# Kernel tuning notes

Measured on AMD Instinct MI355X. Metric: run time of the kernel, lower is better.

The kernel has to match this reference:

```python
import jax, jax.numpy as jnp
import numpy as np

HIDDEN = 1024
NUM_EXPERTS = 16
TOP_K = 6
EPS = 1e-10


def setup_inputs() -> dict:
    key = jax.random.key(0)
    k1, k2, k3, k4 = jax.random.split(key, 4)
    tokens = jax.random.normal(k1, (4, 2048, HIDDEN), dtype=jnp.float32)
    # torch.nn.Linear(hidden_size, num_experts): weight [E, H], bias [E]
    bound = 1.0 / np.sqrt(HIDDEN)
    router_w = jax.random.uniform(k2, (NUM_EXPERTS, HIDDEN), jnp.float32, -bound, bound)
    router_b = jax.random.uniform(k3, (NUM_EXPERTS,), jnp.float32, -bound, bound)
    # expert_weights = randn(E, H, H) / sqrt(H)
    expert_w = jax.random.normal(k4, (NUM_EXPERTS, HIDDEN, HIDDEN), dtype=jnp.float32) / np.sqrt(HIDDEN)
    return {"tokens": tokens, "router_w": router_w, "router_b": router_b, "expert_w": expert_w}


def reference(tokens, router_w, router_b, expert_w):
    B, S, H = tokens.shape
    E = expert_w.shape[0]
    T = B * S

    # Router: softmax -> top-k -> renormalize top-k probs
    logits = jnp.einsum("bsh,eh->bse", tokens, router_w) + router_b  # [B,S,E]
    probs = jax.nn.softmax(logits, axis=-1)
    top_p, top_i = jax.lax.top_k(probs, TOP_K)                        # [B,S,K]
    top_p = top_p / (jnp.sum(top_p, axis=-1, keepdims=True) + EPS)

    x = tokens.reshape(T, H)
    flat_i = top_i.reshape(T, TOP_K)
    flat_p = top_p.reshape(T, TOP_K)

    # Dense gate matrix [T, E]: scatter of normalized top-k weights.
    # Equivalent to the expand/sort/pad + weighted scatter-add restore.
    gate = jnp.zeros((T, E), dtype=flat_p.dtype)
    gate = gate.at[jnp.arange(T)[:, None], flat_i].add(flat_p)
    acc = jnp.maximum(jnp.sum(gate, axis=-1), EPS)  # weight accumulator (clamp min=1e-10)

    # Grouped GEMM equivalent: per-expert matmul weighted by gate, accumulated.
    out = jnp.zeros_like(x)
    for e in range(E):  # fixed, small structural loop over experts
        out = out + (x @ expert_w[e]) * gate[:, e:e + 1]
    out = (out / acc[:, None]).reshape(B, S, H)

    # 'dummy' gradient-connection term from restore_output_with_triton_and_gradients
    out = out + EPS * jnp.sum(top_p, axis=-1, keepdims=True)
    return out
```

## Files before the change

kernel.cpp:

```cpp
#include <hip/hip_runtime.h>
#include <cstdint>
#include <cstddef>

#define NE 16
#define TOPK 6
#define HID 1024
#define NTOK 8192
#define EPSF 1e-10f
#define CAP_ROWS 51200
#define MAXB256 208
#define NT 16
#define ROUTER_BLKS 2048

typedef short bf16x8 __attribute__((ext_vector_type(8)));
typedef float f32x4 __attribute__((ext_vector_type(4)));

__device__ __forceinline__ unsigned int f2bf_rne(float f) {
  union { float f; unsigned int u; } v;
  v.f = f;
  return (v.u + 0x7FFFu + ((v.u >> 16) & 1u)) >> 16;
}

__device__ __forceinline__ float bfbits2f(unsigned int hi16) {
  union { unsigned int u; float f; } v;
  v.u = hi16 << 16;
  return v.f;
}

__device__ __forceinline__ void load_lds16(const void* g, void* l) {
  __builtin_amdgcn_global_load_lds(
      (const __attribute__((address_space(1))) void*)g,
      (__attribute__((address_space(3))) void*)l, 16, 0, 0);
}

__global__ __launch_bounds__(256) void fused_pre_kernel(
    const float* __restrict__ tokens, const float* __restrict__ rw,
    const float* __restrict__ rb, unsigned short* __restrict__ Xb,
    unsigned int* __restrict__ topk, float* __restrict__ g6,
    float* __restrict__ epst, const float* __restrict__ ew,
    unsigned short* __restrict__ wt) {
  __shared__ float tile[64][65];
  const int tid = threadIdx.x;
  const unsigned bx = blockIdx.x;

  if (bx >= ROUTER_BLKS) {
    const int q = bx - ROUTER_BLKS;
    const int e2 = q >> 8;
    const int ntile = ((q >> 4) & 15) * 64;
    const int ktile = (q & 15) * 64;
    const int tr = tid >> 6;
    const int tc = tid & 63;
    const float* wp = ew + (size_t)e2 * HID * HID;
#pragma unroll
    for (int r = 0; r < 64; r += 4)
      tile[r + tr][tc] = wp[(size_t)(ktile + r + tr) * HID + ntile + tc];
    __syncthreads();
    unsigned short* wo = wt + (size_t)e2 * HID * HID;
    const int aa = tid & 31;
    const int rg = tid >> 5;
#pragma unroll
    for (int c2 = 0; c2 < 64; c2 += 8) {
      const int n = c2 + rg;
      const unsigned lo = f2bf_rne(tile[2 * aa][n]);
      const unsigned hi = f2bf_rne(tile[2 * aa + 1][n]);
      *(unsigned int*)(wo + (size_t)(ntile + n) * HID + ktile + 2 * aa) =
          lo | (hi << 16);
    }
    return;
  }

  const int wv = tid >> 6;
  const int lane = tid & 63;
  const int token = (int)bx * 4 + wv;

  const float4* xp4 = (const float4*)(tokens + (size_t)token * HID);
  float4 x4[4];
#pragma unroll
  for (int j = 0; j < 4; ++j) x4[j] = xp4[lane + 64 * j];

  unsigned short* xbrow = Xb + (size_t)token * HID;
#pragma unroll
  for (int j = 0; j < 4; ++j) {
    const unsigned lo = f2bf_rne(x4[j].x) | (f2bf_rne(x4[j].y) << 16);
    const unsigned hi = f2bf_rne(x4[j].z) | (f2bf_rne(x4[j].w) << 16);
    *(uint2*)(xbrow + 4 * (lane + 64 * j)) = (uint2){lo, hi};
  }

  float lg[NE];
#pragma unroll
  for (int e = 0; e < NE; ++e) {
    const float4* wp4 = (const float4*)(rw + e * HID);
    float p = 0.f;
#pragma unroll
    for (int j = 0; j < 4; ++j) {
      const float4 w = wp4[lane + 64 * j];
      p += x4[j].x * w.x + x4[j].y * w.y + x4[j].z * w.z + x4[j].w * w.w;
    }
    lg[e] = p;
  }
#pragma unroll
  for (int m = 1; m < 64; m <<= 1) {
#pragma unroll
    for (int e = 0; e < NE; ++e) lg[e] += __shfl_xor(lg[e], m);
  }
  float mx = -1e30f;
#pragma unroll
  for (int e = 0; e < NE; ++e) {
    lg[e] += rb[e];
    mx = fmaxf(mx, lg[e]);
  }
  float q[NE];
  float s_all = 0.f;
#pragma unroll
  for (int e = 0; e < NE; ++e) {
    q[e] = expf(lg[e] - mx);
    s_all += q[e];
  }
  unsigned sel = 0, pack = 0;
  float s_top = 0.f;
  float gq[TOPK];
#pragma unroll
  for (int k = 0; k < TOPK; ++k) {
    float best = -1.f;
    int bi = 0;
#pragma unroll
    for (int e = 0; e < NE; ++e) {
      bool taken = (sel >> e) & 1u;
      if (!taken && q[e] > best) { best = q[e]; bi = e; }
    }
    sel |= 1u << bi;
    gq[k] = best;
    s_top += best;
    pack |= ((unsigned)bi) << (4 * k);
  }
  if (lane < TOPK)
    g6[(size_t)token * TOPK + lane] = gq[lane] / s_top;
  if (lane == 32) {
    topk[token] = pack;
    float s = s_top / s_all;
    epst[token] = EPSF * (s / (s + EPSF));
  }
}

__global__ __launch_bounds__(1024) void sortassign_kernel(
    const unsigned int* __restrict__ topk, const float* __restrict__ g6,
    unsigned int* __restrict__ tokmap, float* __restrict__ gpos,
    unsigned int* __restrict__ inv, unsigned int* __restrict__ table,
    unsigned int* __restrict__ total) {
  __shared__ unsigned int sred[NE][65];
  __shared__ unsigned int s_seg[NE];
  __shared__ unsigned int hist[NE];
  __shared__ unsigned int s_sc[1024];
  const int e = blockIdx.x;
  const int tid = threadIdx.x;

  {
    const unsigned hx = tid & 15u;
    const int hc = tid >> 4;
    const unsigned int* tp = topk + hc * 128;
    unsigned hcnt = 0;
    for (int i = 0; i < 128; ++i) {
      const unsigned p = tp[i];
#pragma unroll
      for (int k = 0; k < TOPK; ++k) hcnt += (((p >> (4 * k)) & 15u) == hx);
    }
    sred[hx][hc] = hcnt;
  }
  __syncthreads();
  if (tid < NE) {
    unsigned s = 0;
    for (int j = 0; j < 64; ++j) s += sred[tid][j];
    hist[tid] = s;
  }
  __syncthreads();
  if (tid == 0) {
    unsigned off = 0;
    for (int i = 0; i < NE; ++i) {
      s_seg[i] = off;
      off += ((hist[i] + 127) >> 7) << 7;
    }
  }
  __syncthreads();
  if (e == 0 && tid == 0) {
    unsigned b = 0;
    for (int i = 0; i < NE; ++i) {
      const unsigned nb = (hist[i] + 127) >> 7;
      const unsigned seg = s_seg[i];
      unsigned m = 0;
      for (; m + 2 <= nb; m += 2)
        table[b++] = ((unsigned)i << 24) | (seg + m * 128);
      if (m < nb)
        table[b++] = ((unsigned)i << 24) | (1u << 23) | (seg + m * 128);
    }
    *total = b;
  }

  const int tbase = tid * (NTOK / 1024);
  unsigned c = 0;
  for (int i = 0; i < NTOK / 1024; ++i) {
    const unsigned p = topk[tbase + i];
#pragma unroll
    for (int k = 0; k < TOPK; ++k) c += (((p >> (4 * k)) & 15u) == (unsigned)e);
  }
  s_sc[tid] = c;
  __syncthreads();
  for (int off = 1; off < 1024; off <<= 1) {
    unsigned v = (tid >= off) ? s_sc[tid - off] : 0u;
    __syncthreads();
    s_sc[tid] += v;
    __syncthreads();
  }
  const unsigned seg0 = s_seg[e];
  unsigned pos = seg0 + s_sc[tid] - c;
  for (int i = 0; i < NTOK / 1024; ++i) {
    const int t = tbase + i;
    const unsigned p = topk[t];
#pragma unroll
    for (int k = 0; k < TOPK; ++k) {
      if (((p >> (4 * k)) & 15u) == (unsigned)e) {
        tokmap[pos] = (unsigned)t;
        gpos[pos] = g6[(size_t)t * TOPK + k];
        inv[(size_t)t * TOPK + k] = pos;
        ++pos;
      }
    }
  }
  const unsigned cnt_e = s_sc[1023];
  const unsigned segend = seg0 + (((cnt_e + 127) >> 7) << 7);
  for (unsigned p2 = seg0 + cnt_e + tid; p2 < segend; p2 += 1024) {
    tokmap[p2] = 0u;
    gpos[p2] = 0.f;
  }
}

__global__ __launch_bounds__(512, 2) void moe_ggemm_kernel(
    const unsigned short* __restrict__ Xb, const unsigned short* __restrict__ Wt,
    const unsigned int* __restrict__ table, const unsigned int* __restrict__ total,
    const unsigned int* __restrict__ tokmap, const float* __restrict__ gpos,
    unsigned short* __restrict__ Y) {
  __shared__ unsigned short As[2][256][64];
  __shared__ unsigned short Bs[2][256][64];
  __shared__ unsigned int Ts[256];
  __shared__ float Gs[256];

  const unsigned tot = *total;
  const unsigned bx = blockIdx.x;
  const unsigned wg = (bx & 7u) * (MAXB256 * 4u / 8u) + (bx >> 3);
  const unsigned slot = wg >> 2;
  if (slot >= tot) return;
  const int n0 = (int)(wg & 3u) * 256;
  const unsigned ent = table[slot];
  const int e = (int)(ent >> 24);
  const int half = (int)((ent >> 23) & 1u);
  const int row0 = (int)(ent & 0x7FFFFFu);

  const int tid = threadIdx.x;
  const int wv = tid >> 6;
  const int lane = tid & 63;
  const int lm = lane & 15;
  const int quad = lane >> 4;
  const int wvm = wv >> 2;
  const int woff_m = wvm * 128;
  const int woff_n = (wv & 3) * 64;

  if (tid < 256) {
    const int rc = (half && tid >= 128) ? 127 : tid;
    Ts[tid] = tokmap[row0 + rc];
    Gs[tid] = (half && tid >= 128) ? 0.f : gpos[row0 + rc];
  }
  __syncthreads();

  const int srow = tid >> 3;
  const int scol = ((tid & 7) ^ (srow & 7)) << 4;
  const char* pA[4];
  const char* pB[4];
#pragma unroll
  for (int i = 0; i < 4; ++i) {
    pA[i] = (const char*)Xb + (size_t)Ts[i * 64 + srow] * (HID * 2) + scol;
    pB[i] = (const char*)Wt + (size_t)e * (HID * HID * 2) +
            (size_t)(n0 + i * 64 + srow) * (HID * 2) + scol;
  }
  char* const Ab = (char*)&As[0][0][0];
  char* const Bb = (char*)&Bs[0][0][0];
  const int sdst = wv * 8 * 128;

  load_lds16(pA[0], Ab + 0 * 8192 + sdst);
  load_lds16(pA[2], Ab + 2 * 8192 + sdst);
  load_lds16(pB[0], Bb + 0 * 8192 + sdst);
  load_lds16(pB[1], Bb + 1 * 8192 + sdst);
  load_lds16(pB[2], Bb + 2 * 8192 + sdst);
  load_lds16(pB[3], Bb + 3 * 8192 + sdst);
  load_lds16(pA[1], Ab + 1 * 8192 + sdst);
  load_lds16(pA[3], Ab + 3 * 8192 + sdst);

  f32x4 acc[8][4];
#pragma unroll
  for (int f = 0; f < 8; ++f)
#pragma unroll
    for (int g = 0; g < 4; ++g) acc[f][g] = (f32x4){0.f, 0.f, 0.f, 0.f};

  const int rsw = (lm & 7) << 4;
  const int roff0 = (quad * 16) ^ rsw;
  const int roff1 = (64 + quad * 16) ^ rsw;

  asm volatile("s_waitcnt vmcnt(2)" ::: "memory");
  __builtin_amdgcn_s_barrier();

  for (int kt = 0; kt < NT; ++kt) {
    const int c = kt & 1;
    const int koff = (kt < NT - 1 ? kt + 1 : kt) * 128;
    const char* ab = Ab + c * 32768;
    const char* bb = Bb + c * 32768;
    char* const ast = Ab + (c ^ 1) * 32768;
    char* const bst = Bb + (c ^ 1) * 32768;

    bf16x8 a[4][2], b[4][2];

#pragma unroll
    for (int f = 0; f < 4; ++f) {
      const char* rp = ab + (woff_m + 16 * f + lm) * 128;
      a[f][0] = *(const bf16x8*)(rp + roff0);
      a[f][1] = *(const bf16x8*)(rp + roff1);
    }
#pragma unroll
    for (int g = 0; g < 2; ++g) {
      const char* rp = bb + (woff_n + 16 * g + lm) * 128;
      b[g][0] = *(const bf16x8*)(rp + roff0);
      b[g][1] = *(const bf16x8*)(rp + roff1);
    }
    load_lds16(pA[0] + koff, ast + 0 * 8192 + sdst);
    load_lds16(pA[2] + koff, ast + 2 * 8192 + sdst);
    __builtin_amdgcn_s_barrier();
    asm volatile("s_waitcnt lgkmcnt(0)" ::: "memory");
    __builtin_amdgcn_s_setprio(1);
#pragma unroll
    for (int f = 0; f < 4; ++f)
#pragma unroll
      for (int g = 0; g < 2; ++g) {
        acc[f][g] = __builtin_amdgcn_mfma_f32_16x16x32_bf16(a[f][0], b[g][0], acc[f][g], 0, 0, 0);
        acc[f][g] = __builtin_amdgcn_mfma_f32_16x16x32_bf16(a[f][1], b[g][1], acc[f][g], 0, 0, 0);
      }
    __builtin_amdgcn_s_setprio(0);
    __builtin_amdgcn_s_barrier();

#pragma unroll
    for (int g = 2; g < 4; ++g) {
      const char* rp = bb + (woff_n + 16 * g + lm) * 128;
      b[g][0] = *(const bf16x8*)(rp + roff0);
      b[g][1] = *(const bf16x8*)(rp + roff1);
    }
    load_lds16(pB[0] + koff, bst + 0 * 8192 + sdst);
    load_lds16(pB[1] + koff, bst + 1 * 8192 + sdst);
    __builtin_amdgcn_s_barrier();
    asm volatile("s_waitcnt lgkmcnt(0)" ::: "memory");
    __builtin_amdgcn_s_setprio(1);
#pragma unroll
    for (int f = 0; f < 4; ++f)
#pragma unroll
      for (int g = 2; g < 4; ++g) {
        acc[f][g] = __builtin_amdgcn_mfma_f32_16x16x32_bf16(a[f][0], b[g][0], acc[f][g], 0, 0, 0);
        acc[f][g] = __builtin_amdgcn_mfma_f32_16x16x32_bf16(a[f][1], b[g][1], acc[f][g], 0, 0, 0);
      }
    __builtin_amdgcn_s_setprio(0);
    asm volatile("s_waitcnt vmcnt(4)" ::: "memory");
    __builtin_amdgcn_s_barrier();

#pragma unroll
    for (int f = 0; f < 4; ++f) {
      const char* rp = ab + (woff_m + 16 * (f + 4) + lm) * 128;
      a[f][0] = *(const bf16x8*)(rp + roff0);
      a[f][1] = *(const bf16x8*)(rp + roff1);
    }
    load_lds16(pB[2] + koff, bst + 2 * 8192 + sdst);
    load_lds16(pB[3] + koff, bst + 3 * 8192 + sdst);
    __builtin_amdgcn_s_barrier();
    asm volatile("s_waitcnt lgkmcnt(0)" ::: "memory");
    __builtin_amdgcn_s_setprio(1);
#pragma unroll
    for (int f = 0; f < 4; ++f)
#pragma unroll
      for (int g = 2; g < 4; ++g) {
        acc[f + 4][g] = __builtin_amdgcn_mfma_f32_16x16x32_bf16(a[f][0], b[g][0], acc[f + 4][g], 0, 0, 0);
        acc[f + 4][g] = __builtin_amdgcn_mfma_f32_16x16x32_bf16(a[f][1], b[g][1], acc[f + 4][g], 0, 0, 0);
      }
    __builtin_amdgcn_s_setprio(0);
    __builtin_amdgcn_s_barrier();

    load_lds16(pA[1] + koff, ast + 1 * 8192 + sdst);
    load_lds16(pA[3] + koff, ast + 3 * 8192 + sdst);
    __builtin_amdgcn_s_barrier();
    __builtin_amdgcn_s_setprio(1);
#pragma unroll
    for (int f = 0; f < 4; ++f)
#pragma unroll
      for (int g = 0; g < 2; ++g) {
        acc[f + 4][g] = __builtin_amdgcn_mfma_f32_16x16x32_bf16(a[f][0], b[g][0], acc[f + 4][g], 0, 0, 0);
        acc[f + 4][g] = __builtin_amdgcn_mfma_f32_16x16x32_bf16(a[f][1], b[g][1], acc[f + 4][g], 0, 0, 0);
      }
    __builtin_amdgcn_s_setprio(0);
    asm volatile("s_waitcnt vmcnt(2)" ::: "memory");
    __builtin_amdgcn_s_barrier();
  }

  asm volatile("s_waitcnt vmcnt(0)" ::: "memory");

  if (!(half && wvm)) {
#pragma unroll
    for (int f = 0; f < 8; ++f)
#pragma unroll
      for (int r = 0; r < 4; ++r) {
        const int row = woff_m + 16 * f + quad * 4 + r;
        const float gte = Gs[row];
        unsigned short* yrow = Y + (size_t)(row0 + row) * HID + n0;
#pragma unroll
        for (int g = 0; g < 4; ++g)
          yrow[woff_n + 16 * g + lm] = (unsigned short)f2bf_rne(gte * acc[f][g][r]);
      }
  }
}

__global__ __launch_bounds__(256) void reduce_kernel(
    const unsigned short* __restrict__ Y, const unsigned int* __restrict__ inv,
    const float* __restrict__ epst, float* __restrict__ out) {
  const int sub = threadIdx.x >> 7;
  const int ct = threadIdx.x & 127;
  const int t = blockIdx.x * 2 + sub;
  const int c0 = ct * 8;

  float s[8];
  const float ep = epst[t];
#pragma unroll
  for (int i = 0; i < 8; ++i) s[i] = ep;

#pragma unroll
  for (int k = 0; k < TOPK; ++k) {
    const unsigned pos = inv[(size_t)t * TOPK + k];
    const uint4 v = *(const uint4*)(Y + (size_t)pos * HID + c0);
    s[0] += bfbits2f(v.x & 0xFFFFu);
    s[1] += bfbits2f(v.x >> 16);
    s[2] += bfbits2f(v.y & 0xFFFFu);
    s[3] += bfbits2f(v.y >> 16);
    s[4] += bfbits2f(v.z & 0xFFFFu);
    s[5] += bfbits2f(v.z >> 16);
    s[6] += bfbits2f(v.w & 0xFFFFu);
    s[7] += bfbits2f(v.w >> 16);
  }
  float* orow = out + (size_t)t * HID + c0;
  *(float4*)orow = (float4){s[0], s[1], s[2], s[3]};
  *(float4*)(orow + 4) = (float4){s[4], s[5], s[6], s[7]};
}

extern "C" void kernel_launch(void* const* d_in, const int* in_sizes, int n_in,
                              void* d_out, int out_size, void* d_ws, size_t ws_size,
                              hipStream_t stream) {
  const float* tokens = (const float*)d_in[0];
  const float* rw = (const float*)d_in[1];
  const float* rb = (const float*)d_in[2];
  const float* ew = (const float*)d_in[3];
  float* out = (float*)d_out;

  char* ws = (char*)d_ws;
  const size_t OFF_XB = 0;
  const size_t OFF_WT = 16777216;
  const size_t OFF_Y = 50331648;
  const size_t OFF_META = 155189248;
  const size_t M_TOKMAP = OFF_META + 0;
  const size_t M_GPOS = OFF_META + 204800;
  const size_t M_TOTAL = OFF_META + 409600;
  const size_t M_TABLE = OFF_META + 409664;
  const size_t M_INV = OFF_META + 411328;
  const size_t M_TOPK = OFF_META + 607936;
  const size_t M_G6 = OFF_META + 640704;
  const size_t M_EPST = OFF_META + 837312;

  unsigned short* Xb = (unsigned short*)(ws + OFF_XB);
  unsigned short* Wt = (unsigned short*)(ws + OFF_WT);
  unsigned short* Y = (unsigned short*)(ws + OFF_Y);
  unsigned int* tokmap = (unsigned int*)(ws + M_TOKMAP);
  float* gpos = (float*)(ws + M_GPOS);
  unsigned int* total = (unsigned int*)(ws + M_TOTAL);
  unsigned int* table = (unsigned int*)(ws + M_TABLE);
  unsigned int* inv = (unsigned int*)(ws + M_INV);
  unsigned int* topk = (unsigned int*)(ws + M_TOPK);
  float* g6 = (float*)(ws + M_G6);
  float* epst = (float*)(ws + M_EPST);

  fused_pre_kernel<<<dim3(ROUTER_BLKS + (HID / 64) * (HID / 64) * NE), dim3(256),
                     0, stream>>>(tokens, rw, rb, Xb, topk, g6, epst, ew, Wt);
  sortassign_kernel<<<dim3(NE), dim3(1024), 0, stream>>>(
      topk, g6, tokmap, gpos, inv, table, total);
  moe_ggemm_kernel<<<dim3(MAXB256 * 4), dim3(512), 0, stream>>>(
      Xb, Wt, table, total, tokmap, gpos, Y);
  reduce_kernel<<<dim3(NTOK / 2), dim3(256), 0, stream>>>(Y, inv, epst, out);
}
```

Measured before the change: 343.1 us.

## Make grouped GEMM persistent with cross-tile prefetch; use wave-shuffle scan in sort

The grouped GEMM now launches 256 persistent workgroups, each working through a contiguous per-XCD range of tiles. On the last k-step of one tile it prefetches the first k-slice of the next tile, so the pipeline prologue no longer stalls at tile boundaries and the per-block setup cost is paid less often. The sort kernel replaces its 1024-wide LDS Hillis-Steele scan, which needed many barriers, with wave shuffles plus a small per-wave offset pass. It also takes the expert count from the histogram. The persistent schedule can leave load imbalance across blocks, and the tile epilogue now sits serially between tiles.

```diff
diff --git a/kernel.cpp b/kernel.cpp
--- a/kernel.cpp
+++ b/kernel.cpp
@@ -150,9 +150,11 @@
   __shared__ unsigned int sred[NE][65];
   __shared__ unsigned int s_seg[NE];
   __shared__ unsigned int hist[NE];
-  __shared__ unsigned int s_sc[1024];
+  __shared__ unsigned int wofs[16];
   const int e = blockIdx.x;
   const int tid = threadIdx.x;
+  const int lane = tid & 63;
+  const int wvid = tid >> 6;
 
   {
     const unsigned hx = tid & 15u;
@@ -169,7 +171,7 @@
   __syncthreads();
   if (tid < NE) {
     unsigned s = 0;
-    for (int j = 0; j < 64; ++j) s += sred[tid][j];
+    for (int jj = 0; jj < 64; ++jj) s += sred[tid][jj];
     hist[tid] = s;
   }
   __syncthreads();
@@ -179,20 +181,19 @@
       s_seg[i] = off;
       off += ((hist[i] + 127) >> 7) << 7;
     }
-  }
-  __syncthreads();
-  if (e == 0 && tid == 0) {
-    unsigned b = 0;
-    for (int i = 0; i < NE; ++i) {
-      const unsigned nb = (hist[i] + 127) >> 7;
-      const unsigned seg = s_seg[i];
-      unsigned m = 0;
-      for (; m + 2 <= nb; m += 2)
-        table[b++] = ((unsigned)i << 24) | (seg + m * 128);
-      if (m < nb)
-        table[b++] = ((unsigned)i << 24) | (1u << 23) | (seg + m * 128);
-    }
-    *total = b;
+    if (e == 0) {
+      unsigned b = 0;
+      for (int i = 0; i < NE; ++i) {
+        const unsigned nb = (hist[i] + 127) >> 7;
+        const unsigned seg = s_seg[i];
+        unsigned m = 0;
+        for (; m + 2 <= nb; m += 2)
+          table[b++] = ((unsigned)i << 24) | (seg + m * 128);
+        if (m < nb)
+          table[b++] = ((unsigned)i << 24) | (1u << 23) | (seg + m * 128);
+      }
+      *total = b;
+    }
   }
 
   const int tbase = tid * (NTOK / 1024);
@@ -202,16 +203,22 @@
 #pragma unroll
     for (int k = 0; k < TOPK; ++k) c += (((p >> (4 * k)) & 15u) == (unsigned)e);
   }
-  s_sc[tid] = c;
+  unsigned pfx = c;
+#pragma unroll
+  for (int m = 1; m < 64; m <<= 1) {
+    const unsigned v = __shfl_up(pfx, m);
+    if (lane >= m) pfx += v;
+  }
+  if (lane == 63) wofs[wvid] = pfx;
   __syncthreads();
-  for (int off = 1; off < 1024; off <<= 1) {
-    unsigned v = (tid >= off) ? s_sc[tid - off] : 0u;
-    __syncthreads();
-    s_sc[tid] += v;
-    __syncthreads();
-  }
+  if (tid == 0) {
+    unsigned r = 0;
+    for (int i = 0; i < 16; ++i) { const unsigned t = wofs[i]; wofs[i] = r; r += t; }
+  }
+  __syncthreads();
+
   const unsigned seg0 = s_seg[e];
-  unsigned pos = seg0 + s_sc[tid] - c;
+  unsigned pos = seg0 + wofs[wvid] + (pfx - c);
   for (int i = 0; i < NTOK / 1024; ++i) {
     const int t = tbase + i;
     const unsigned p = topk[t];
@@ -225,7 +232,7 @@
       }
     }
   }
-  const unsigned cnt_e = s_sc[1023];
+  const unsigned cnt_e = hist[e];
   const unsigned segend = seg0 + (((cnt_e + 127) >> 7) << 7);
   for (unsigned p2 = seg0 + cnt_e + tid; p2 < segend; p2 += 1024) {
     tokmap[p2] = 0u;
@@ -240,21 +247,24 @@
     unsigned short* __restrict__ Y) {
   __shared__ unsigned short As[2][256][64];
   __shared__ unsigned short Bs[2][256][64];
-  __shared__ unsigned int Ts[256];
   __shared__ float Gs[256];
-
+  __shared__ unsigned int Stab[MAXB256];
+
+  const int tid = threadIdx.x;
   const unsigned tot = *total;
+  if (tid < MAXB256) Stab[tid] = table[tid];
+  __syncthreads();
+
+  const unsigned nwg = tot * 4u;
   const unsigned bx = blockIdx.x;
-  const unsigned wg = (bx & 7u) * (MAXB256 * 4u / 8u) + (bx >> 3);
-  const unsigned slot = wg >> 2;
-  if (slot >= tot) return;
-  const int n0 = (int)(wg & 3u) * 256;
-  const unsigned ent = table[slot];
-  const int e = (int)(ent >> 24);
-  const int half = (int)((ent >> 23) & 1u);
-  const int row0 = (int)(ent & 0x7FFFFFu);
-
-  const int tid = threadIdx.x;
+  const unsigned xcd = bx & 7u;
+  const unsigned jj = bx >> 3;
+  const unsigned chunk = (nwg + 7u) >> 3;
+  const unsigned wbeg = xcd * chunk + jj;
+  unsigned wend = (xcd + 1u) * chunk;
+  if (wend > nwg) wend = nwg;
+  if (wbeg >= wend) return;
+
   const int wv = tid >> 6;
   const int lane = tid & 63;
   const int lm = lane & 15;
@@ -262,27 +272,36 @@
   const int wvm = wv >> 2;
   const int woff_m = wvm * 128;
   const int woff_n = (wv & 3) * 64;
-
-  if (tid < 256) {
-    const int rc = (half && tid >= 128) ? 127 : tid;
-    Ts[tid] = tokmap[row0 + rc];
-    Gs[tid] = (half && tid >= 128) ? 0.f : gpos[row0 + rc];
-  }
-  __syncthreads();
-
   const int srow = tid >> 3;
   const int scol = ((tid & 7) ^ (srow & 7)) << 4;
-  const char* pA[4];
-  const char* pB[4];
-#pragma unroll
-  for (int i = 0; i < 4; ++i) {
-    pA[i] = (const char*)Xb + (size_t)Ts[i * 64 + srow] * (HID * 2) + scol;
-    pB[i] = (const char*)Wt + (size_t)e * (HID * HID * 2) +
-            (size_t)(n0 + i * 64 + srow) * (HID * 2) + scol;
-  }
+  const int rsw = (lm & 7) << 4;
+  const int roff0 = (quad * 16) ^ rsw;
+  const int roff1 = (64 + quad * 16) ^ rsw;
   char* const Ab = (char*)&As[0][0][0];
   char* const Bb = (char*)&Bs[0][0][0];
   const int sdst = wv * 8 * 128;
+
+  unsigned w = wbeg;
+  unsigned ent = Stab[w >> 2];
+  int half = (int)((ent >> 23) & 1u);
+  int row0 = (int)(ent & 0x7FFFFFu);
+  int n0 = (int)(w & 3u) * 256;
+  const char* pA[4];
+  const char* pB[4];
+  {
+    const int e = (int)(ent >> 24);
+#pragma unroll
+    for (int i = 0; i < 4; ++i) {
+      const int r = i * 64 + srow;
+      const int rc = (half && r >= 128) ? 127 : r;
+      pA[i] = (const char*)Xb + (size_t)tokmap[row0 + rc] * (HID * 2) + scol;
+      pB[i] = (const char*)Wt + (size_t)e * (HID * HID * 2) +
+              (size_t)(n0 + i * 64 + srow) * (HID * 2) + scol;
+    }
+  }
+  if (tid < 256)
+    Gs[tid] = gpos[row0 + ((half && tid >= 128) ? 127 : tid)];
+  __syncthreads();
 
   load_lds16(pA[0], Ab + 0 * 8192 + sdst);
   load_lds16(pA[2], Ab + 2 * 8192 + sdst);
@@ -299,124 +318,169 @@
 #pragma unroll
     for (int g = 0; g < 4; ++g) acc[f][g] = (f32x4){0.f, 0.f, 0.f, 0.f};
 
-  const int rsw = (lm & 7) << 4;
-  const int roff0 = (quad * 16) ^ rsw;
-  const int roff1 = (64 + quad * 16) ^ rsw;
-
   asm volatile("s_waitcnt vmcnt(2)" ::: "memory");
   __builtin_amdgcn_s_barrier();
 
-  for (int kt = 0; kt < NT; ++kt) {
-    const int c = kt & 1;
-    const int koff = (kt < NT - 1 ? kt + 1 : kt) * 128;
-    const char* ab = Ab + c * 32768;
-    const char* bb = Bb + c * 32768;
-    char* const ast = Ab + (c ^ 1) * 32768;
-    char* const bst = Bb + (c ^ 1) * 32768;
-
-    bf16x8 a[4][2], b[4][2];
-
-#pragma unroll
-    for (int f = 0; f < 4; ++f) {
-      const char* rp = ab + (woff_m + 16 * f + lm) * 128;
-      a[f][0] = *(const bf16x8*)(rp + roff0);
-      a[f][1] = *(const bf16x8*)(rp + roff1);
-    }
-#pragma unroll
-    for (int g = 0; g < 2; ++g) {
-      const char* rp = bb + (woff_n + 16 * g + lm) * 128;
-      b[g][0] = *(const bf16x8*)(rp + roff0);
-      b[g][1] = *(const bf16x8*)(rp + roff1);
-    }
-    load_lds16(pA[0] + koff, ast + 0 * 8192 + sdst);
-    load_lds16(pA[2] + koff, ast + 2 * 8192 + sdst);
-    __builtin_amdgcn_s_barrier();
-    asm volatile("s_waitcnt lgkmcnt(0)" ::: "memory");
-    __builtin_amdgcn_s_setprio(1);
-#pragma unroll
-    for (int f = 0; f < 4; ++f)
+  while (true) {
+    const unsigned wn = (w + 32u < wend) ? w + 32u : w;
+    const unsigned ent2 = Stab[wn >> 2];
+    const int half2 = (int)((ent2 >> 23) & 1u);
+    const int row02 = (int)(ent2 & 0x7FFFFFu);
+    const int n02 = (int)(wn & 3u) * 256;
+    const char* nA[4];
+    const char* nB[4];
+    {
+      const int e2 = (int)(ent2 >> 24);
+#pragma unroll
+      for (int i = 0; i < 4; ++i) {
+        const int r = i * 64 + srow;
+        const int rc = (half2 && r >= 128) ? 127 : r;
+        nA[i] = (const char*)Xb + (size_t)tokmap[row02 + rc] * (HID * 2) + scol;
+        nB[i] = (const char*)Wt + (size_t)e2 * (HID * HID * 2) +
+                (size_t)(n02 + i * 64 + srow) * (HID * 2) + scol;
+      }
+    }
+    float g2val = 0.f;
+    if (tid < 256)
+      g2val = gpos[row02 + ((half2 && tid >= 128) ? 127 : tid)];
+
+    for (int kt = 0; kt < NT; ++kt) {
+      const int c = kt & 1;
+      const char* ab = Ab + c * 32768;
+      const char* bb = Bb + c * 32768;
+      char* const ast = Ab + (c ^ 1) * 32768;
+      char* const bst = Bb + (c ^ 1) * 32768;
+
+      const char *sA0, *sA1, *sA2, *sA3, *sB0, *sB1, *sB2, *sB3;
+      if (kt < NT - 1) {
+        const int koff = (kt + 1) * 128;
+        sA0 = pA[0] + koff; sA1 = pA[1] + koff;
+        sA2 = pA[2] + koff; sA3 = pA[3] + koff;
+        sB0 = pB[0] + koff; sB1 = pB[1] + koff;
+        sB2 = pB[2] + koff; sB3 = pB[3] + koff;
+      } else {
+        sA0 = nA[0]; sA1 = nA[1]; sA2 = nA[2]; sA3 = nA[3];
+        sB0 = nB[0]; sB1 = nB[1]; sB2 = nB[2]; sB3 = nB[3];
+      }
+
+      bf16x8 a[4][2], b[4][2];
+
+#pragma unroll
+      for (int f = 0; f < 4; ++f) {
+        const char* rp = ab + (woff_m + 16 * f + lm) * 128;
+        a[f][0] = *(const bf16x8*)(rp + roff0);
+        a[f][1] = *(const bf16x8*)(rp + roff1);
+      }
 #pragma unroll
       for (int g = 0; g < 2; ++g) {
-        acc[f][g] = __builtin_amdgcn_mfma_f32_16x16x32_bf16(a[f][0], b[g][0], acc[f][g], 0, 0, 0);
-        acc[f][g] = __builtin_amdgcn_mfma_f32_16x16x32_bf16(a[f][1], b[g][1], acc[f][g], 0, 0, 0);
-      }
-    __builtin_amdgcn_s_setprio(0);
-    __builtin_amdgcn_s_barrier();
-
-#pragma unroll
-    for (int g = 2; g < 4; ++g) {
-      const char* rp = bb + (woff_n + 16 * g + lm) * 128;
-      b[g][0] = *(const bf16x8*)(rp + roff0);
-      b[g][1] = *(const bf16x8*)(rp + roff1);
-    }
-    load_lds16(pB[0] + koff, bst + 0 * 8192 + sdst);
-    load_lds16(pB[1] + koff, bst + 1 * 8192 + sdst);
-    __builtin_amdgcn_s_barrier();
-    asm volatile("s_waitcnt lgkmcnt(0)" ::: "memory");
-    __builtin_amdgcn_s_setprio(1);
-#pragma unroll
-    for (int f = 0; f < 4; ++f)
+        const char* rp = bb + (woff_n + 16 * g + lm) * 128;
+        b[g][0] = *(const bf16x8*)(rp + roff0);
+        b[g][1] = *(const bf16x8*)(rp + roff1);
+      }
+      load_lds16(sA0, ast + 0 * 8192 + sdst);
+      load_lds16(sA2, ast + 2 * 8192 + sdst);
+      __builtin_amdgcn_s_barrier();
+      asm volatile("s_waitcnt lgkmcnt(0)" ::: "memory");
+      __builtin_amdgcn_s_setprio(1);
+#pragma unroll
+      for (int f = 0; f < 4; ++f)
+#pragma unroll
+        for (int g = 0; g < 2; ++g) {
+          acc[f][g] = __builtin_amdgcn_mfma_f32_16x16x32_bf16(a[f][0], b[g][0], acc[f][g], 0, 0, 0);
+          acc[f][g] = __builtin_amdgcn_mfma_f32_16x16x32_bf16(a[f][1], b[g][1], acc[f][g], 0, 0, 0);
+        }
+      __builtin_amdgcn_s_setprio(0);
+      __builtin_amdgcn_s_barrier();
+
 #pragma unroll
       for (int g = 2; g < 4; ++g) {
-        acc[f][g] = __builtin_amdgcn_mfma_f32_16x16x32_bf16(a[f][0], b[g][0], acc[f][g], 0, 0, 0);
-        acc[f][g] = __builtin_amdgcn_mfma_f32_16x16x32_bf16(a[f][1], b[g][1], acc[f][g], 0, 0, 0);
-      }
-    __builtin_amdgcn_s_setprio(0);
-    asm volatile("s_waitcnt vmcnt(4)" ::: "memory");
-    __builtin_amdgcn_s_barrier();
-
-#pragma unroll
-    for (int f = 0; f < 4; ++f) {
-      const char* rp = ab + (woff_m + 16 * (f + 4) + lm) * 128;
-      a[f][0] = *(const bf16x8*)(rp + roff0);
-      a[f][1] = *(const bf16x8*)(rp + roff1);
-    }
-    load_lds16(pB[2] + koff, bst + 2 * 8192 + sdst);
-    load_lds16(pB[3] + koff, bst + 3 * 8192 + sdst);
-    __builtin_amdgcn_s_barrier();
-    asm volatile("s_waitcnt lgkmcnt(0)" ::: "memory");
-    __builtin_amdgcn_s_setprio(1);
-#pragma unroll
-    for (int f = 0; f < 4; ++f)
-#pragma unroll
-      for (int g = 2; g < 4; ++g) {
-        acc[f + 4][g] = __builtin_amdgcn_mfma_f32_16x16x32_bf16(a[f][0], b[g][0], acc[f + 4][g], 0, 0, 0);
-        acc[f + 4][g] = __builtin_amdgcn_mfma_f32_16x16x32_bf16(a[f][1], b[g][1], acc[f + 4][g], 0, 0, 0);
-      }
-    __builtin_amdgcn_s_setprio(0);
-    __builtin_amdgcn_s_barrier();
-
-    load_lds16(pA[1] + koff, ast + 1 * 8192 + sdst);
-    load_lds16(pA[3] + koff, ast + 3 * 8192 + sdst);
-    __builtin_amdgcn_s_barrier();
-    __builtin_amdgcn_s_setprio(1);
-#pragma unroll
-    for (int f = 0; f < 4; ++f)
-#pragma unroll
-      for (int g = 0; g < 2; ++g) {
-        acc[f + 4][g] = __builtin_amdgcn_mfma_f32_16x16x32_bf16(a[f][0], b[g][0], acc[f + 4][g], 0, 0, 0);
-        acc[f + 4][g] = __builtin_amdgcn_mfma_f32_16x16x32_bf16(a[f][1], b[g][1], acc[f + 4][g], 0, 0, 0);
-      }
-    __builtin_amdgcn_s_setprio(0);
-    asm volatile("s_waitcnt vmcnt(2)" ::: "memory");
-    __builtin_amdgcn_s_barrier();
+        const char* rp = bb + (woff_n + 16 * g + lm) * 128;
+        b[g][0] = *(const bf16x8*)(rp + roff0);
+        b[g][1] = *(const bf16x8*)(rp + roff1);
+      }
+      load_lds16(sB0, bst + 0 * 8192 + sdst);
+      load_lds16(sB1, bst + 1 * 8192 + sdst);
+      __builtin_amdgcn_s_barrier();
+      asm volatile("s_waitcnt lgkmcnt(0)" ::: "memory");
+      __builtin_amdgcn_s_setprio(1);
+#pragma unroll
+      for (int f = 0; f < 4; ++f)
+#pragma unroll
+        for (int g = 2; g < 4; ++g) {
+          acc[f][g] = __builtin_amdgcn_mfma_f32_16x16x32_bf16(a[f][0], b[g][0], acc[f][g], 0, 0, 0);
+          acc[f][g] = __builtin_amdgcn_mfma_f32_16x16x32_bf16(a[f][1], b[g][1], acc[f][g], 0, 0, 0);
+        }
+      __builtin_amdgcn_s_setprio(0);
+      asm volatile("s_waitcnt vmcnt(4)" ::: "memory");
+      __builtin_amdgcn_s_barrier();
+
+#pragma unroll
+      for (int f = 0; f < 4; ++f) {
+        const char* rp = ab + (woff_m + 16 * (f + 4) + lm) * 128;
+        a[f][0] = *(const bf16x8*)(rp + roff0);
+        a[f][1] = *(const bf16x8*)(rp + roff1);
+      }
+      load_lds16(sB2, bst + 2 * 8192 + sdst);
+      load_lds16(sB3, bst + 3 * 8192 + sdst);
+      __builtin_amdgcn_s_barrier();
+      asm volatile("s_waitcnt lgkmcnt(0)" ::: "memory");
+      __builtin_amdgcn_s_setprio(1);
+#pragma unroll
+      for (int f = 0; f < 4; ++f)
+#pragma unroll
+        for (int g = 2; g < 4; ++g) {
+          acc[f + 4][g] = __builtin_amdgcn_mfma_f32_16x16x32_bf16(a[f][0], b[g][0], acc[f + 4][g], 0, 0, 0);
+          acc[f + 4][g] = __builtin_amdgcn_mfma_f32_16x16x32_bf16(a[f][1], b[g][1], acc[f + 4][g], 0, 0, 0);
+        }
+      __builtin_amdgcn_s_setprio(0);
+      __builtin_amdgcn_s_barrier();
+
+      load_lds16(sA1, ast + 1 * 8192 + sdst);
+      load_lds16(sA3, ast + 3 * 8192 + sdst);
+      __builtin_amdgcn_s_barrier();
+      __builtin_amdgcn_s_setprio(1);
+#pragma unroll
+      for (int f = 0; f < 4; ++f)
+#pragma unroll
+        for (int g = 0; g < 2; ++g) {
+          acc[f + 4][g] = __builtin_amdgcn_mfma_f32_16x16x32_bf16(a[f][0], b[g][0], acc[f + 4][g], 0, 0, 0);
+          acc[f + 4][g] = __builtin_amdgcn_mfma_f32_16x16x32_bf16(a[f][1], b[g][1], acc[f + 4][g], 0, 0, 0);
+        }
+      __builtin_amdgcn_s_setprio(0);
+      asm volatile("s_waitcnt vmcnt(2)" ::: "memory");
+      __builtin_amdgcn_s_barrier();
+    }
+
+    if (!(half && wvm)) {
+#pragma unroll
+      for (int f = 0; f < 8; ++f)
+#pragma unroll
+        for (int r = 0; r < 4; ++r) {
+          const int row = woff_m + 16 * f + quad * 4 + r;
+          const float gte = Gs[row];
+          unsigned short* yrow = Y + (size_t)(row0 + row) * HID + n0;
+#pragma unroll
+          for (int g = 0; g < 4; ++g)
+            yrow[woff_n + 16 * g + lm] = (unsigned short)f2bf_rne(gte * acc[f][g][r]);
+        }
+    }
+    __syncthreads();
+    if (tid < 256) Gs[tid] = g2val;
+    if (wn == w) break;
+
+    w = wn;
+    half = half2;
+    row0 = row02;
+    n0 = n02;
+#pragma unroll
+    for (int i = 0; i < 4; ++i) { pA[i] = nA[i]; pB[i] = nB[i]; }
+#pragma unroll
+    for (int f = 0; f < 8; ++f)
+#pragma unroll
+      for (int g = 0; g < 4; ++g) acc[f][g] = (f32x4){0.f, 0.f, 0.f, 0.f};
   }
 
   asm volatile("s_waitcnt vmcnt(0)" ::: "memory");
-
-  if (!(half && wvm)) {
-#pragma unroll
-    for (int f = 0; f < 8; ++f)
-#pragma unroll
-      for (int r = 0; r < 4; ++r) {
-        const int row = woff_m + 16 * f + quad * 4 + r;
-        const float gte = Gs[row];
-        unsigned short* yrow = Y + (size_t)(row0 + row) * HID + n0;
-#pragma unroll
-        for (int g = 0; g < 4; ++g)
-          yrow[woff_n + 16 * g + lm] = (unsigned short)f2bf_rne(gte * acc[f][g][r]);
-      }
-  }
 }
 
 __global__ __launch_bounds__(256) void reduce_kernel(
@@ -489,7 +553,7 @@
                      0, stream>>>(tokens, rw, rb, Xb, topk, g6, epst, ew, Wt);
   sortassign_kernel<<<dim3(NE), dim3(1024), 0, stream>>>(
       topk, g6, tokmap, gpos, inv, table, total);
-  moe_ggemm_kernel<<<dim3(MAXB256 * 4), dim3(512), 0, stream>>>(
+  moe_ggemm_kernel<<<dim3(256), dim3(512), 0, stream>>>(
       Xb, Wt, table, total, tokmap, gpos, Y);
   reduce_kernel<<<dim3(NTOK / 2), dim3(256), 0, stream>>>(Y, inv, epst, out);
 }
```

Measured after the change: 340.7 us. No clear change (-0.7%).
